# Kernel optimization log

Measured on AMD Instinct MI355X. Metric: run time of the kernel, lower is better.

## Reference

```python
import jax, jax.numpy as jnp
import numpy as np

EPS = 1e-12


def _sq_dists(x, y):
    # x: [B, N1, 3], y: [B, N2, 3] -> squared pairwise distances [B, N1, N2]
    x2 = jnp.sum(x * x, axis=-1)            # [B, N1]
    y2 = jnp.sum(y * y, axis=-1)            # [B, N2]
    xy = jnp.einsum('bnd,bmd->bnm', x, y)   # [B, N1, N2]
    d = x2[:, :, None] + y2[:, None, :] - 2.0 * xy
    return jnp.maximum(d, 0.0)


def setup_inputs() -> dict:
    key = jax.random.key(0)
    k1, k2 = jax.random.split(key)
    xyz1 = jax.random.normal(k1, (8, 8192, 3), dtype=jnp.float32)
    xyz2 = jax.random.normal(k2, (8, 8192, 3), dtype=jnp.float32)
    return {"xyz1": xyz1, "xyz2": xyz2}


def reference(xyz1, xyz2):
    d = _sq_dists(xyz1, xyz2)                       # [B, N1, N2]
    dist1 = jnp.min(d, axis=2)                      # nearest in xyz2 for each xyz1 point
    dist2 = jnp.min(d, axis=1)                      # nearest in xyz1 for each xyz2 point
    dist1 = jnp.sqrt(jnp.maximum(dist1, EPS))
    dist2 = jnp.sqrt(jnp.maximum(dist2, EPS))
    per_batch = (jnp.mean(dist1, axis=1) + jnp.mean(dist2, axis=1)) / 2.0  # [B]
    return jnp.mean(per_batch)
```

## Files before the change

### kernel.cpp

```cpp
#include <hip/hip_runtime.h>
#include <math.h>


#define NPTS   8192
#define NB     8
#define NPC    (NB * NPTS)
#define BLOCK  512
#define CHUNK  1024
#define CS     2
#define COLS   (NPTS / CS)
#define TOTALQ (2 * NPC)
#define EPSV   1e-12f

typedef _Float16 v8h  __attribute__((ext_vector_type(8)));
typedef float    v16f __attribute__((ext_vector_type(16)));

__global__ __launch_bounds__(256) void chamfer_prep(
    const float* __restrict__ xyz1, const float* __restrict__ xyz2,
    v8h* __restrict__ form, unsigned* __restrict__ bits)
{
    const int gid = blockIdx.x * 256 + threadIdx.x;
    const float* __restrict__ src = (gid < NPC) ? xyz1 : xyz2;
    const int i = (gid < NPC) ? gid : gid - NPC;
    float x = src[3 * i], y = src[3 * i + 1], z = src[3 * i + 2];
    _Float16 xh = (_Float16)x, yh = (_Float16)y, zh = (_Float16)z;
    float xf = (float)xh, yf = (float)yh, zf = (float)zh;
    float n = fmaf(xf, xf, fmaf(yf, yf, zf * zf));
    v8h bv = {};
    bv[0] = xh; bv[1] = yh; bv[2] = zh;
    bv[3] = (_Float16)n; bv[4] = (_Float16)1.0f;
    form[gid] = bv;
    bits[gid] = 0x7F7F7F7FU;
}

#define MFMA(va, vb) __builtin_amdgcn_mfma_f32_32x32x16_f16((va), (vb), vzero, 0, 0, 0)

__global__ __launch_bounds__(BLOCK, 4) void chamfer_mfma_min(
    const v8h* __restrict__ form, unsigned* __restrict__ bits)
{
    const int bid = blockIdx.x;
    const int cs  = bid & (CS - 1);
    const int rb  = (bid >> 1) & 31;
    const int b   = (bid >> 6) & 7;
    const int dir = (bid >> 9) & 1;

    const v8h* __restrict__ qf = form + (size_t)dir * NPC + (size_t)b * NPTS;
    const v8h* __restrict__ tf = form + (size_t)(1 - dir) * NPC
                                      + (size_t)b * NPTS + cs * COLS;

    const int tid  = threadIdx.x;
    const int lane = tid & 63;
    const int w    = tid >> 6;
    const int c31  = lane & 31;
    const int rowbase = rb * 256;

    v8h a0 = {};
    if (lane < 32) {
        const _Float16 m2 = (_Float16)(-2.0f);
        v8h f = qf[rowbase + w * 32 + lane];
        a0[0] = m2 * f[0]; a0[1] = m2 * f[1]; a0[2] = m2 * f[2];
        a0[3] = (_Float16)1.0f; a0[4] = f[3];
    }

    float rm0[16];
#pragma unroll
    for (int r = 0; r < 16; ++r) rm0[r] = 3.4e38f;

    __shared__ v8h bsh[CHUNK];
    const v16f vzero = {};

    for (int ch = 0; ch < COLS / CHUNK; ++ch) {
        __syncthreads();
        const v8h* __restrict__ g = tf + ch * CHUNK;
#pragma unroll
        for (int k = 0; k < CHUNK / BLOCK; ++k)
            bsh[k * BLOCK + tid] = g[k * BLOCK + tid];
        __syncthreads();

#pragma unroll
        for (int cc = 0; cc < CHUNK / 64; ++cc) {
            const v8h b0 = bsh[cc * 64 + c31];
            const v8h b1 = bsh[cc * 64 + 32 + c31];
            v16f p = MFMA(a0, b0);
            v16f q = MFMA(a0, b1);
#pragma unroll
            for (int r = 0; r < 16; ++r)
                rm0[r] = fminf(fminf(rm0[r], p[r]), q[r]);
        }
    }

    unsigned* dst = bits + (size_t)(dir * NB + b) * NPTS + rowbase;
#pragma unroll
    for (int r = 0; r < 16; ++r) {
        float v = rm0[r];
        v = fminf(v, __shfl_xor(v, 1));
        v = fminf(v, __shfl_xor(v, 2));
        v = fminf(v, __shfl_xor(v, 4));
        v = fminf(v, __shfl_xor(v, 8));
        v = fminf(v, __shfl_xor(v, 16));
        if ((lane & 31) == 0) {
            int row_local = w * 32 + (r & 3) + 8 * (r >> 2) + 4 * (lane >> 5);
            atomicMin(dst + row_local, __float_as_uint(fmaxf(v, 0.0f)));
        }
    }
}

__global__ __launch_bounds__(256) void chamfer_reduce1(
    const unsigned* __restrict__ bits,
    float* __restrict__ sums)
{
    const int idx = blockIdx.x * 256 + threadIdx.x;
    float m = __uint_as_float(bits[idx]);
    float val = sqrtf(fmaxf(m, EPSV));

    __shared__ float red[256];
    red[threadIdx.x] = val;
    __syncthreads();
    for (int s = 128; s > 0; s >>= 1) {
        if (threadIdx.x < s) red[threadIdx.x] += red[threadIdx.x + s];
        __syncthreads();
    }
    if (threadIdx.x == 0) sums[blockIdx.x] = red[0];
}

#define NSUMS (TOTALQ / 256)

__global__ __launch_bounds__(NSUMS) void chamfer_finalize(
    const float* __restrict__ sums, float* __restrict__ out)
{
    __shared__ float red[NSUMS];
    red[threadIdx.x] = sums[threadIdx.x];
    __syncthreads();
    for (int s = NSUMS / 2; s > 0; s >>= 1) {
        if (threadIdx.x < s) red[threadIdx.x] += red[threadIdx.x + s];
        __syncthreads();
    }
    if (threadIdx.x == 0) out[0] = red[0] * (1.0f / (float)TOTALQ);
}

extern "C" void kernel_launch(void* const* d_in, const int* in_sizes, int n_in,
                              void* d_out, int out_size, void* d_ws, size_t ws_size,
                              hipStream_t stream) {
    const float* xyz1 = (const float*)d_in[0];
    const float* xyz2 = (const float*)d_in[1];
    float* out = (float*)d_out;

    v8h*      formbuf = (v8h*)d_ws;
    unsigned* bitsbuf = (unsigned*)(formbuf + TOTALQ);
    float*    sums    = (float*)(bitsbuf + TOTALQ);

    chamfer_prep<<<TOTALQ / 256, 256, 0, stream>>>(xyz1, xyz2, formbuf, bitsbuf);
    chamfer_mfma_min<<<2 * NB * 32 * CS, BLOCK, 0, stream>>>(formbuf, bitsbuf);
    chamfer_reduce1<<<TOTALQ / 256, 256, 0, stream>>>(bitsbuf, sums);
    chamfer_finalize<<<1, NSUMS, 0, stream>>>(sums, out);
}
```

Baseline: 47.19 us.

## Drop column split and fuse sqrt-sum into MFMA kernel with fixed-point atomic

Each block now scans all target columns, so every row minimum is complete inside the block. The sqrt and sum are then done in-kernel, and a block total is added to a single 64-bit fixed-point atomic counter. This removes the per-row atomicMin buffer, its initialisation and the separate reduction kernel. It also adds s_setprio around the MFMA pair. The trade-off is that the grid halves to 512 blocks, which lowers parallelism and doubles per-block work, and the fixed-point conversion adds a small rounding error.

```diff
diff --git a/kernel.cpp b/kernel.cpp
--- a/kernel.cpp
+++ b/kernel.cpp
@@ -7,19 +7,20 @@
 #define NPC    (NB * NPTS)
 #define BLOCK  512
 #define CHUNK  1024
-#define CS     2
-#define COLS   (NPTS / CS)
+#define COLS   NPTS
 #define TOTALQ (2 * NPC)
 #define EPSV   1e-12f
+#define FXSCALE 67108864.0
 
 typedef _Float16 v8h  __attribute__((ext_vector_type(8)));
 typedef float    v16f __attribute__((ext_vector_type(16)));
 
 __global__ __launch_bounds__(256) void chamfer_prep(
     const float* __restrict__ xyz1, const float* __restrict__ xyz2,
-    v8h* __restrict__ form, unsigned* __restrict__ bits)
+    v8h* __restrict__ form, unsigned long long* __restrict__ counter)
 {
     const int gid = blockIdx.x * 256 + threadIdx.x;
+    if (gid == 0) counter[0] = 0ULL;
     const float* __restrict__ src = (gid < NPC) ? xyz1 : xyz2;
     const int i = (gid < NPC) ? gid : gid - NPC;
     float x = src[3 * i], y = src[3 * i + 1], z = src[3 * i + 2];
@@ -30,23 +31,20 @@
     bv[0] = xh; bv[1] = yh; bv[2] = zh;
     bv[3] = (_Float16)n; bv[4] = (_Float16)1.0f;
     form[gid] = bv;
-    bits[gid] = 0x7F7F7F7FU;
 }
 
 #define MFMA(va, vb) __builtin_amdgcn_mfma_f32_32x32x16_f16((va), (vb), vzero, 0, 0, 0)
 
 __global__ __launch_bounds__(BLOCK, 4) void chamfer_mfma_min(
-    const v8h* __restrict__ form, unsigned* __restrict__ bits)
+    const v8h* __restrict__ form, unsigned long long* __restrict__ counter)
 {
     const int bid = blockIdx.x;
-    const int cs  = bid & (CS - 1);
-    const int rb  = (bid >> 1) & 31;
-    const int b   = (bid >> 6) & 7;
-    const int dir = (bid >> 9) & 1;
+    const int rb  = bid & 31;
+    const int b   = (bid >> 5) & 7;
+    const int dir = (bid >> 8) & 1;
 
     const v8h* __restrict__ qf = form + (size_t)dir * NPC + (size_t)b * NPTS;
-    const v8h* __restrict__ tf = form + (size_t)(1 - dir) * NPC
-                                      + (size_t)b * NPTS + cs * COLS;
+    const v8h* __restrict__ tf = form + (size_t)(1 - dir) * NPC + (size_t)b * NPTS;
 
     const int tid  = threadIdx.x;
     const int lane = tid & 63;
@@ -81,15 +79,17 @@
         for (int cc = 0; cc < CHUNK / 64; ++cc) {
             const v8h b0 = bsh[cc * 64 + c31];
             const v8h b1 = bsh[cc * 64 + 32 + c31];
+            __builtin_amdgcn_s_setprio(1);
             v16f p = MFMA(a0, b0);
             v16f q = MFMA(a0, b1);
+            __builtin_amdgcn_s_setprio(0);
 #pragma unroll
             for (int r = 0; r < 16; ++r)
                 rm0[r] = fminf(fminf(rm0[r], p[r]), q[r]);
         }
     }
 
-    unsigned* dst = bits + (size_t)(dir * NB + b) * NPTS + rowbase;
+    float acc = 0.0f;
 #pragma unroll
     for (int r = 0; r < 16; ++r) {
         float v = rm0[r];
@@ -98,44 +98,27 @@
         v = fminf(v, __shfl_xor(v, 4));
         v = fminf(v, __shfl_xor(v, 8));
         v = fminf(v, __shfl_xor(v, 16));
-        if ((lane & 31) == 0) {
-            int row_local = w * 32 + (r & 3) + 8 * (r >> 2) + 4 * (lane >> 5);
-            atomicMin(dst + row_local, __float_as_uint(fmaxf(v, 0.0f)));
-        }
+        if ((lane & 31) == 0)
+            acc += sqrtf(fmaxf(fmaxf(v, 0.0f), EPSV));
+    }
+    acc += __shfl_xor(acc, 32);
+
+    __syncthreads();
+    float* red = (float*)bsh;
+    if (lane == 0) red[w] = acc;
+    __syncthreads();
+    if (tid == 0) {
+        float s = red[0] + red[1] + red[2] + red[3]
+                + red[4] + red[5] + red[6] + red[7];
+        unsigned long long fx = (unsigned long long)((double)s * FXSCALE + 0.5);
+        atomicAdd(counter, fx);
     }
 }
 
-__global__ __launch_bounds__(256) void chamfer_reduce1(
-    const unsigned* __restrict__ bits,
-    float* __restrict__ sums)
+__global__ void chamfer_finalize(
+    const unsigned long long* __restrict__ counter, float* __restrict__ out)
 {
-    const int idx = blockIdx.x * 256 + threadIdx.x;
-    float m = __uint_as_float(bits[idx]);
-    float val = sqrtf(fmaxf(m, EPSV));
-
-    __shared__ float red[256];
-    red[threadIdx.x] = val;
-    __syncthreads();
-    for (int s = 128; s > 0; s >>= 1) {
-        if (threadIdx.x < s) red[threadIdx.x] += red[threadIdx.x + s];
-        __syncthreads();
-    }
-    if (threadIdx.x == 0) sums[blockIdx.x] = red[0];
-}
-
-#define NSUMS (TOTALQ / 256)
-
-__global__ __launch_bounds__(NSUMS) void chamfer_finalize(
-    const float* __restrict__ sums, float* __restrict__ out)
-{
-    __shared__ float red[NSUMS];
-    red[threadIdx.x] = sums[threadIdx.x];
-    __syncthreads();
-    for (int s = NSUMS / 2; s > 0; s >>= 1) {
-        if (threadIdx.x < s) red[threadIdx.x] += red[threadIdx.x + s];
-        __syncthreads();
-    }
-    if (threadIdx.x == 0) out[0] = red[0] * (1.0f / (float)TOTALQ);
+    out[0] = (float)((double)counter[0] * (1.0 / FXSCALE) / (double)TOTALQ);
 }
 
 extern "C" void kernel_launch(void* const* d_in, const int* in_sizes, int n_in,
@@ -145,12 +128,10 @@
     const float* xyz2 = (const float*)d_in[1];
     float* out = (float*)d_out;
 
-    v8h*      formbuf = (v8h*)d_ws;
-    unsigned* bitsbuf = (unsigned*)(formbuf + TOTALQ);
-    float*    sums    = (float*)(bitsbuf + TOTALQ);
+    v8h* formbuf = (v8h*)d_ws;
+    unsigned long long* counter = (unsigned long long*)(formbuf + TOTALQ);
 
-    chamfer_prep<<<TOTALQ / 256, 256, 0, stream>>>(xyz1, xyz2, formbuf, bitsbuf);
-    chamfer_mfma_min<<<2 * NB * 32 * CS, BLOCK, 0, stream>>>(formbuf, bitsbuf);
-    chamfer_reduce1<<<TOTALQ / 256, 256, 0, stream>>>(bitsbuf, sums);
-    chamfer_finalize<<<1, NSUMS, 0, stream>>>(sums, out);
+    chamfer_prep<<<TOTALQ / 256, 256, 0, stream>>>(xyz1, xyz2, formbuf, counter);
+    chamfer_mfma_min<<<2 * NB * 32, BLOCK, 0, stream>>>(formbuf, counter);
+    chamfer_finalize<<<1, 1, 0, stream>>>(counter, out);
 }
```

Result: no change. 46.56 us (-1.3%).
